# Kernel tuning notes

Hardware: AMD Instinct MI355X
Metric: run time of the kernel (lower is better)

## Reference

```python
import jax, jax.numpy as jnp
import numpy as np

ALPHA = 4.0   # spikingjelly sigmoid surrogate alpha
TAU = 2.0
EPS = 1e-5
NUM_HEADS = 8

@jax.custom_vjp
def spike(x):
    return (x >= 0.0).astype(x.dtype)

def _spike_fwd(x):
    return spike(x), x

def _spike_bwd(x, g):
    s = jax.nn.sigmoid(ALPHA * x)
    return (g * ALPHA * s * (1.0 - s),)

spike.defvjp(_spike_fwd, _spike_bwd)

def lif(x):
    # Multi-step LIF over leading time axis T; hard reset to 0, detach_reset=True.
    def step(v, xt):
        h = v + (xt - v) / TAU
        s = spike(h - 1.0)
        v_new = (1.0 - jax.lax.stop_gradient(s)) * h
        return v_new, s
    _, out = jax.lax.scan(step, jnp.zeros_like(x[0]), x)
    return out

def bn(x, gamma, beta):
    # x: (T*B, N, D). torch applies BatchNorm1d on (T*B, D, N): per-channel-D
    # batch stats over (T*B, N) dims (training mode, biased var).
    mean = x.mean(axis=(0, 1))
    var = x.var(axis=(0, 1))
    return (x - mean) * jax.lax.rsqrt(var + EPS) * gamma + beta

def proximity_mask(T):
    # assumed create_temporal_proximity_mask: weight decays with |i-j|
    idx = jnp.arange(T)
    return 1.0 / (1.0 + jnp.abs(idx[:, None] - idx[None, :]).astype(jnp.float32))

def _branch(x, W, g, b, T, B, H, d):
    D = H * d
    y = bn(x.reshape(T * B, -1, D) @ W.T, g, b)
    return lif(y.reshape(T, B, -1, H, d))  # (T,B,N,H,d)

def _forward(q, kv, Wq, gq, bq, Wk, gk, bk, Wv, gv, bv, Wp, gp, bp):
    T, B, N, D = q.shape
    H = NUM_HEADS
    d = D // H
    scale = D ** (-0.5)
    mask = proximity_mask(T)  # (T,T)

    qh = _branch(q, Wq, gq, bq, T, B, H, d)   # (T,B,N,H,d)
    kh = _branch(kv, Wk, gk, bk, T, B, H, d)  # (T,B,N,H,d)
    vh = _branch(kv, Wv, gv, bv, T, B, H, d)  # (T,B,N,H,d)

    # torch: k,v transposed over (time, token) axes before matmul.
    # scores[x,b,h,i,j] = sum_d q[x,b,i,h,d] * k[j,b,x,h,d]
    scores = jnp.einsum('xbihd,jbxhd->xbhij', qh, kh)
    scores = scores * mask[None, None, None, :, :]
    # z[x,b,h,i,d] = sum_j scores[x,b,h,i,j] * v[j,b,x,h,d]
    z = jnp.einsum('xbhij,jbxhd->xbhid', scores, vh) * scale

    # permute(3,1,0,2,4) -> (i=N, B, x=T, H, d); reshape to (T,B,T,D)
    z = z.transpose(3, 1, 0, 2, 4).reshape(T, B, T, D)
    z = lif(z)  # attn_lif

    y = z.reshape(T * B, T, D) @ Wp.T
    y = bn(y, gp, bp).reshape(T, B, T, D)
    y = lif(y)  # proj_lif; dropout is identity (eval)
    return y

def setup_inputs() -> dict:
    T, B, N, D = 64, 8, 64, 384
    key = jax.random.key(0)
    ks = jax.random.split(key, 6)
    w = lambda k: (jax.random.normal(k, (D, D), dtype=jnp.float32) * 0.02)
    return {
        'q': jax.random.normal(ks[0], (T, B, N, D), dtype=jnp.float32),
        'kv': jax.random.normal(ks[1], (T, B, N, D), dtype=jnp.float32),
        'Wq': w(ks[2]), 'gq': jnp.ones((D,), jnp.float32), 'bq': jnp.zeros((D,), jnp.float32),
        'Wk': w(ks[3]), 'gk': jnp.ones((D,), jnp.float32), 'bk': jnp.zeros((D,), jnp.float32),
        'Wv': w(ks[4]), 'gv': jnp.ones((D,), jnp.float32), 'bv': jnp.zeros((D,), jnp.float32),
        'Wp': w(ks[5]), 'gp': jnp.ones((D,), jnp.float32), 'bp': jnp.zeros((D,), jnp.float32),
    }

def reference(q, kv, Wq, gq, bq, Wk, gk, bk, Wv, gv, bv, Wp, gp, bp):
    return _forward(q, kv, Wq, gq, bq, Wk, gk, bk, Wv, gv, bv, Wp, gp, bp)
```

## Files before the change

kernel.cpp:

```cpp
#include <hip/hip_runtime.h>

typedef unsigned char u8;
typedef unsigned short u16;
typedef unsigned int u32;
typedef unsigned long long u64;
typedef __attribute__((ext_vector_type(8))) short s16x8;
typedef __attribute__((ext_vector_type(4))) float f32x4;

#define T_DIM 64
#define B_DIM 8
#define N_DIM 64
#define D_DIM 384
#define H_DIM 8
#define HD 48
#define M_ROWS 32768
#define CH 196608
#define STATS_BLOCKS 256

#define IMG_PER_KSTEP 16384
#define IMG_PER_NTILE (12 * IMG_PER_KSTEP)
#define IMG_PER_W (3 * IMG_PER_NTILE)

__device__ __forceinline__ void split8(const float* e, int4& o1, int4& o2, int4& o3) {
  u16 h1[8], h2[8], h3[8];
#pragma unroll
  for (int i = 0; i < 8; ++i) {
    const float x = e[i];
    const u32 b = __float_as_uint(x);
    h1[i] = (u16)(b >> 16);
    const float x1 = __uint_as_float(b & 0xFFFF0000u);
    const float r1 = x - x1;
    const u32 c = __float_as_uint(r1);
    h2[i] = (u16)(c >> 16);
    const float x2 = __uint_as_float(c & 0xFFFF0000u);
    const float r2 = r1 - x2;
    h3[i] = (u16)(__float_as_uint(r2) >> 16);
  }
  o1 = make_int4((int)((u32)h1[0] | ((u32)h1[1] << 16)), (int)((u32)h1[2] | ((u32)h1[3] << 16)),
                 (int)((u32)h1[4] | ((u32)h1[5] << 16)), (int)((u32)h1[6] | ((u32)h1[7] << 16)));
  o2 = make_int4((int)((u32)h2[0] | ((u32)h2[1] << 16)), (int)((u32)h2[2] | ((u32)h2[3] << 16)),
                 (int)((u32)h2[4] | ((u32)h2[5] << 16)), (int)((u32)h2[6] | ((u32)h2[7] << 16)));
  o3 = make_int4((int)((u32)h3[0] | ((u32)h3[1] << 16)), (int)((u32)h3[2] | ((u32)h3[3] << 16)),
                 (int)((u32)h3[4] | ((u32)h3[5] << 16)), (int)((u32)h3[6] | ((u32)h3[7] << 16)));
}

__device__ __forceinline__ void split8_2(const float* e, int4& o1, int4& o2) {
  u16 h1[8], h2[8];
#pragma unroll
  for (int i = 0; i < 8; ++i) {
    const float x = e[i];
    const u32 b = __float_as_uint(x);
    h1[i] = (u16)(b >> 16);
    const float x1 = __uint_as_float(b & 0xFFFF0000u);
    const float r1 = x - x1;
    h2[i] = (u16)(__float_as_uint(r1) >> 16);
  }
  o1 = make_int4((int)((u32)h1[0] | ((u32)h1[1] << 16)), (int)((u32)h1[2] | ((u32)h1[3] << 16)),
                 (int)((u32)h1[4] | ((u32)h1[5] << 16)), (int)((u32)h1[6] | ((u32)h1[7] << 16)));
  o2 = make_int4((int)((u32)h2[0] | ((u32)h2[1] << 16)), (int)((u32)h2[2] | ((u32)h2[3] << 16)),
                 (int)((u32)h2[4] | ((u32)h2[5] << 16)), (int)((u32)h2[6] | ((u32)h2[7] << 16)));
}

__device__ __forceinline__ void split1(float xx, u16& a, u16& b2, u16& c) {
  const u32 u = __float_as_uint(xx);
  a = (u16)(u >> 16);
  const float x1 = __uint_as_float(u & 0xFFFF0000u);
  const float r1 = xx - x1;
  const u32 u2 = __float_as_uint(r1);
  b2 = (u16)(u2 >> 16);
  const float x2 = __uint_as_float(u2 & 0xFFFF0000u);
  const float r2 = r1 - x2;
  c = (u16)(__float_as_uint(r2) >> 16);
}

__device__ __forceinline__ u64 packmask48(const u8* p) {
  const int4 r0 = ((const int4*)p)[0];
  const int4 r1 = ((const int4*)p)[1];
  const int4 r2 = ((const int4*)p)[2];
  u32 wv[12] = {(u32)r0.x, (u32)r0.y, (u32)r0.z, (u32)r0.w,
                (u32)r1.x, (u32)r1.y, (u32)r1.z, (u32)r1.w,
                (u32)r2.x, (u32)r2.y, (u32)r2.z, (u32)r2.w};
  u64 bits = 0;
#pragma unroll
  for (int w = 0; w < 12; ++w) {
    const u32 u = wv[w];
    const u32 nib = (u & 1u) | ((u >> 7) & 2u) | ((u >> 14) & 4u) | ((u >> 21) & 8u);
    bits |= (u64)nib << (w * 4);
  }
  return bits;
}

__global__ __launch_bounds__(256) void prep_w(const float* __restrict__ W0,
                                              const float* __restrict__ W1,
                                              const float* __restrict__ W2,
                                              const float* __restrict__ W3,
                                              char* __restrict__ img) {
  const int widx = blockIdx.x & 3;
  const int nt = blockIdx.x >> 2;
  const float* W = (widx == 0) ? W0 : (widx == 1) ? W1 : (widx == 2) ? W2 : W3;
  char* base = img + (size_t)widx * IMG_PER_W + (size_t)nt * IMG_PER_NTILE;
  const int tid = threadIdx.x;
  const int nr = tid >> 1;
  const int kh = tid & 1;
  for (int ks = 0; ks < 12; ++ks) {
    const float* src = W + (size_t)(nt * 128 + nr) * D_DIM + ks * 32 + kh * 16;
    float4 v0 = ((const float4*)src)[0];
    float4 v1 = ((const float4*)src)[1];
    float4 v2 = ((const float4*)src)[2];
    float4 v3 = ((const float4*)src)[3];
    float e[16] = {v0.x, v0.y, v0.z, v0.w, v1.x, v1.y, v1.z, v1.w,
                   v2.x, v2.y, v2.z, v2.w, v3.x, v3.y, v3.z, v3.w};
    int4* dst = (int4*)(base + (size_t)ks * IMG_PER_KSTEP);
#pragma unroll
    for (int sub = 0; sub < 2; ++sub) {
      const int kc = kh * 2 + sub;
      int4 o1, o2, o3;
      split8(e + sub * 8, o1, o2, o3);
      dst[(0 * 4 + kc) * 128 + (nr ^ kc)] = o1;
      dst[(1 * 4 + kc) * 128 + (nr ^ kc)] = o2;
    }
  }
}

template <int ASPL>
__global__ __launch_bounds__(256) void gemm_bn(const void* __restrict__ Ain,
                                               const char* __restrict__ imgW,
                                               float* __restrict__ C,
                                               double* __restrict__ part) {
  constexpr int ABYTES = ASPL * 8192;
  __shared__ __align__(16) char shraw[ABYTES + 16384];
  int4* AchW = (int4*)shraw;
  int4* BchW = (int4*)(shraw + ABYTES);
  const s16x8* AchR = (const s16x8*)shraw;
  const s16x8* BchR = (const s16x8*)(shraw + ABYTES);

  const int tid = threadIdx.x;
  const int lane = tid & 63;
  const int w = tid >> 6;
  const int wm = w >> 1, wn = w & 1;
  const int lr = lane & 15;
  const int kcL = lane >> 4;

  const int wgid = blockIdx.x;
  const int xcdSlot = wgid & 7;
  const int inner = wgid >> 3;
  const int ntx = inner % 3;
  const int by = (inner / 3) * 8 + xcdSlot;
  const int bn = ntx * 128;
  const int bm = by * 128;

  const int4* imgI = (const int4*)(imgW + (size_t)ntx * IMG_PER_NTILE);

  int axc[4], bxc[4];
#pragma unroll
  for (int f = 0; f < 4; ++f) {
    axc[f] = kcL * 128 + ((wm * 64 + f * 16 + lr) ^ kcL);
    bxc[f] = kcL * 128 + ((wn * 64 + f * 16 + lr) ^ kcL);
  }

  float4 a0, a1, a2, a3;
  int4 za0, za1;
  int4 b0, b1, b2, b3;

  const int arow = tid >> 1, akh = tid & 1;
  const int c0 = tid, c1 = tid + 256;

#define LOADA(ks)                                                             \
  do {                                                                        \
    if (ASPL == 2) {                                                          \
      const float* ap = (const float*)Ain + (size_t)(bm + arow) * D_DIM +     \
                        (ks) * 32 + akh * 16;                                 \
      a0 = ((const float4*)ap)[0]; a1 = ((const float4*)ap)[1];               \
      a2 = ((const float4*)ap)[2]; a3 = ((const float4*)ap)[3];               \
    } else {                                                                  \
      const u16* zp = (const u16*)Ain;                                        \
      { const int kc = c0 >> 7, mp = c0 & 127;                                \
        za0 = *(const int4*)(zp + (size_t)(bm + (mp ^ kc)) * D_DIM +          \
                             (ks) * 32 + kc * 8); }                           \
      { const int kc = c1 >> 7, mp = c1 & 127;                                \
        za1 = *(const int4*)(zp + (size_t)(bm + (mp ^ kc)) * D_DIM +          \
                             (ks) * 32 + kc * 8); }                           \
    }                                                                         \
  } while (0)

#define LOADB(ks)                                                             \
  do {                                                                        \
    b0 = imgI[(ks) * 1024 + tid];                                             \
    b1 = imgI[(ks) * 1024 + tid + 256];                                       \
    b2 = imgI[(ks) * 1024 + tid + 512];                                       \
    b3 = imgI[(ks) * 1024 + tid + 768];                                       \
  } while (0)

#define WRITES()                                                              \
  do {                                                                        \
    if (ASPL == 2) {                                                          \
      float e0[8] = {a0.x, a0.y, a0.z, a0.w, a1.x, a1.y, a1.z, a1.w};         \
      float e1[8] = {a2.x, a2.y, a2.z, a2.w, a3.x, a3.y, a3.z, a3.w};         \
      int4 o1, o2;                                                            \
      { const int kc = akh * 2;                                               \
        split8_2(e0, o1, o2);                                                 \
        AchW[0 * 512 + kc * 128 + (arow ^ kc)] = o1;                          \
        AchW[1 * 512 + kc * 128 + (arow ^ kc)] = o2; }                        \
      { const int kc = akh * 2 + 1;                                           \
        split8_2(e1, o1, o2);                                                 \
        AchW[0 * 512 + kc * 128 + (arow ^ kc)] = o1;                          \
        AchW[1 * 512 + kc * 128 + (arow ^ kc)] = o2; }                        \
    } else {                                                                  \
      AchW[c0] = za0; AchW[c1] = za1;                                         \
    }                                                                         \
    BchW[tid] = b0; BchW[tid + 256] = b1;                                     \
    BchW[tid + 512] = b2; BchW[tid + 768] = b3;                               \
  } while (0)

  f32x4 acc[4][4] = {};

  LOADA(0); LOADB(0);
  WRITES();
  __syncthreads();

  for (int ks = 0; ks < 12; ++ks) {
    if (ks < 11) { LOADA(ks + 1); LOADB(ks + 1); }
    s16x8 af[ASPL][4];
#pragma unroll
    for (int s = 0; s < ASPL; ++s)
#pragma unroll
      for (int fm = 0; fm < 4; ++fm) af[s][fm] = AchR[s * 512 + axc[fm]];
#pragma unroll
    for (int fn = 0; fn < 4; ++fn) {
      const s16x8 bf0 = BchR[bxc[fn]];
      const s16x8 bf1 = BchR[512 + bxc[fn]];
      if (ASPL == 2) {
#pragma unroll
        for (int fm = 0; fm < 4; ++fm)
          acc[fm][fn] = __builtin_amdgcn_mfma_f32_16x16x32_bf16(af[ASPL - 1][fm], bf0, acc[fm][fn], 0, 0, 0);
      }
#pragma unroll
      for (int fm = 0; fm < 4; ++fm)
        acc[fm][fn] = __builtin_amdgcn_mfma_f32_16x16x32_bf16(af[0][fm], bf1, acc[fm][fn], 0, 0, 0);
#pragma unroll
      for (int fm = 0; fm < 4; ++fm)
        acc[fm][fn] = __builtin_amdgcn_mfma_f32_16x16x32_bf16(af[0][fm], bf0, acc[fm][fn], 0, 0, 0);
    }
    __syncthreads();
    if (ks < 11) { WRITES(); __syncthreads(); }
  }
#undef LOADA
#undef LOADB
#undef WRITES

#pragma unroll
  for (int fm = 0; fm < 4; ++fm)
#pragma unroll
    for (int fn = 0; fn < 4; ++fn) {
      const int row = bm + wm * 64 + fm * 16 + kcL * 4;
      const int col = bn + wn * 64 + fn * 16 + lr;
#pragma unroll
      for (int r = 0; r < 4; ++r)
        C[(size_t)(row + r) * D_DIM + col] = acc[fm][fn][r];
    }

  double* red = (double*)shraw;
#pragma unroll
  for (int fn = 0; fn < 4; ++fn) {
    const int col = wn * 64 + fn * 16 + lr;
    const int rg = wm * 4 + kcL;
    double s = 0.0, qd = 0.0;
#pragma unroll
    for (int fm = 0; fm < 4; ++fm)
#pragma unroll
      for (int r = 0; r < 4; ++r) {
        const double v = (double)acc[fm][fn][r];
        s += v;
        qd += v * v;
      }
    red[(rg * 128 + col) * 2 + 0] = s;
    red[(rg * 128 + col) * 2 + 1] = qd;
  }
  __syncthreads();
  if (tid < 128) {
    double S = 0.0, Q = 0.0;
#pragma unroll
    for (int rg = 0; rg < 8; ++rg) {
      S += red[(rg * 128 + tid) * 2 + 0];
      Q += red[(rg * 128 + tid) * 2 + 1];
    }
    const size_t pidx = ((size_t)by * D_DIM + bn + tid) * 2;
    part[pidx + 0] = S;
    part[pidx + 1] = Q;
  }
}

__global__ void bn_stats_final(const double* __restrict__ part,
                               const float* __restrict__ gamma,
                               const float* __restrict__ beta,
                               float* __restrict__ ss) {
  const int c = blockIdx.x * 64 + threadIdx.x;
  double s = 0.0, q = 0.0;
  for (int b = 0; b < STATS_BLOCKS; ++b) {
    s += part[((size_t)b * D_DIM + c) * 2 + 0];
    q += part[((size_t)b * D_DIM + c) * 2 + 1];
  }
  const double n = (double)M_ROWS;
  const double mean = s / n;
  const double var = q / n - mean * mean;
  const double rstd = 1.0 / sqrt(var + 1e-5);
  const double sc = (double)gamma[c] * rstd;
  ss[c * 2 + 0] = (float)sc;
  ss[c * 2 + 1] = (float)((double)beta[c] - mean * sc);
}

template <int MODE>
__global__ __launch_bounds__(256) void lif_kernel(float* Y,
                                                  const float* __restrict__ ss,
                                                  u8* __restrict__ spikes) {
  const int c = blockIdx.x * 256 + threadIdx.x;
  const int dd = c % D_DIM;
  const float scale = ss[dd * 2 + 0];
  const float shift = ss[dd * 2 + 1];
  float v = 0.0f;
  for (int t0 = 0; t0 < T_DIM; t0 += 8) {
    float xs[8];
#pragma unroll
    for (int u = 0; u < 8; ++u) xs[u] = Y[(size_t)(t0 + u) * CH + c];
#pragma unroll
    for (int u = 0; u < 8; ++u) {
      const float xv = xs[u] * scale + shift;
      const float hh = v + (xv - v) * 0.5f;
      const float sp = (hh >= 1.0f) ? 1.0f : 0.0f;
      v = (1.0f - sp) * hh;
      if (MODE == 0)
        spikes[(size_t)(t0 + u) * CH + c] = (u8)sp;
      else
        Y[(size_t)(t0 + u) * CH + c] = sp;
    }
  }
}

__global__ __launch_bounds__(256) void attn_kernel(const u8* __restrict__ qs,
                                                   const u8* __restrict__ ks,
                                                   const u8* __restrict__ vs,
                                                   u16* __restrict__ z) {
  const int gid = blockIdx.x;
  const int hg = (gid & 1) * 4;
  const int b = (gid >> 1) & 7;
  const int x = gid >> 4;
  const int w = threadIdx.x >> 6;
  const int h = hg + w;
  const int lane = threadIdx.x & 63;

  union Slab {
    struct { u64 qm[64]; u64 km[64]; float maskT[64]; u16 vt[48][80]; } a;
    float zl[64][50];
  };
  __shared__ Slab sh[4];
  Slab& S = sh[w];

  {
    const u8* qp = qs + ((size_t)((x * B_DIM + b) * N_DIM + lane)) * D_DIM + h * HD;
    S.a.qm[lane] = packmask48(qp);
    const size_t koff = ((size_t)((lane * B_DIM + b) * N_DIM + x)) * D_DIM + h * HD;
    S.a.km[lane] = packmask48(ks + koff);
    const u8* vp = vs + koff;
    const int4 r0 = ((const int4*)vp)[0];
    const int4 r1 = ((const int4*)vp)[1];
    const int4 r2 = ((const int4*)vp)[2];
    u32 vw[12] = {(u32)r0.x, (u32)r0.y, (u32)r0.z, (u32)r0.w,
                  (u32)r1.x, (u32)r1.y, (u32)r1.z, (u32)r1.w,
                  (u32)r2.x, (u32)r2.y, (u32)r2.z, (u32)r2.w};
#pragma unroll
    for (int ww = 0; ww < 12; ++ww) {
      const u32 u = vw[ww];
#pragma unroll
      for (int e = 0; e < 4; ++e)
        S.a.vt[ww * 4 + e][lane] = ((u >> (8 * e)) & 1u) ? (u16)0x3F80 : (u16)0;
    }
    S.a.maskT[lane] = 1.0f / (float)(1 + lane);
  }
  __syncthreads();

  const int lr = lane & 15;
  const int lg = lane >> 4;
  f32x4 acc[4][3] = {};

  for (int ksi = 0; ksi < 2; ++ksi) {
    const int j0 = lg * 8 + ksi * 32;
    s16x8 bf[3];
#pragma unroll
    for (int nf = 0; nf < 3; ++nf)
      bf[nf] = *(const s16x8*)&S.a.vt[lr + nf * 16][j0];
    s16x8 af[3][4];
#pragma unroll
    for (int mf = 0; mf < 4; ++mf) {
      const int i = lr + mf * 16;
      const u64 qi = S.a.qm[i];
      union { u32 w[4]; s16x8 v; } p1, p2, p3;
#pragma unroll
      for (int pp = 0; pp < 4; ++pp) {
        u16 aa[2], bb[2], cc[2];
#pragma unroll
        for (int e = 0; e < 2; ++e) {
          const int j = j0 + pp * 2 + e;
          const int cnt = __popcll(qi & S.a.km[j]);
          int ad = i - j;
          if (ad < 0) ad = -ad;
          const float sv = (float)cnt * S.a.maskT[ad];
          split1(sv, aa[e], bb[e], cc[e]);
        }
        p1.w[pp] = (u32)aa[0] | ((u32)aa[1] << 16);
        p2.w[pp] = (u32)bb[0] | ((u32)bb[1] << 16);
        p3.w[pp] = (u32)cc[0] | ((u32)cc[1] << 16);
      }
      af[0][mf] = p1.v;
      af[1][mf] = p2.v;
      af[2][mf] = p3.v;
    }
#pragma unroll
    for (int spi = 0; spi < 3; ++spi) {
      const int sp = 2 - spi;
#pragma unroll
      for (int nf = 0; nf < 3; ++nf)
#pragma unroll
        for (int mf = 0; mf < 4; ++mf)
          acc[mf][nf] = __builtin_amdgcn_mfma_f32_16x16x32_bf16(af[sp][mf], bf[nf],
                                                                acc[mf][nf], 0, 0, 0);
    }
  }
  __syncthreads();

  const float kScale = 0.05103103630798287f;
#pragma unroll
  for (int mf = 0; mf < 4; ++mf)
#pragma unroll
    for (int nf = 0; nf < 3; ++nf)
#pragma unroll
      for (int r = 0; r < 4; ++r)
        S.zl[mf * 16 + lg * 4 + r][lr + nf * 16] = acc[mf][nf][r] * kScale;
  __syncthreads();

  if (lane < HD) {
    float v = 0.0f;
    for (int i0 = 0; i0 < 64; i0 += 8) {
      float zv[8];
#pragma unroll
      for (int u = 0; u < 8; ++u) zv[u] = S.zl[i0 + u][lane];
#pragma unroll
      for (int u = 0; u < 8; ++u) {
        const float hh = v + (zv[u] - v) * 0.5f;
        const u16 sp16 = (hh >= 1.0f) ? (u16)0x3F80 : (u16)0;
        v = (hh >= 1.0f) ? 0.0f : hh;
        z[((size_t)(((i0 + u) * B_DIM + b) * T_DIM + x)) * D_DIM + h * HD + lane] = sp16;
      }
    }
  }
}

extern "C" void kernel_launch(void* const* d_in, const int* in_sizes, int n_in,
                              void* d_out, int out_size, void* d_ws, size_t ws_size,
                              hipStream_t stream) {
  const float* q  = (const float*)d_in[0];
  const float* kv = (const float*)d_in[1];
  const float* Wq = (const float*)d_in[2];
  const float* gq = (const float*)d_in[3];
  const float* bq = (const float*)d_in[4];
  const float* Wk = (const float*)d_in[5];
  const float* gk = (const float*)d_in[6];
  const float* bk = (const float*)d_in[7];
  const float* Wv = (const float*)d_in[8];
  const float* gv = (const float*)d_in[9];
  const float* bv = (const float*)d_in[10];
  const float* Wp = (const float*)d_in[11];
  const float* gp = (const float*)d_in[12];
  const float* bp = (const float*)d_in[13];
  float* out = (float*)d_out;
  char* ws = (char*)d_ws;

  float* Ybuf  = (float*)(ws + 0);
  u16*   Zb    = (u16*)(ws + 0);
  double* part = (double*)(ws + 50331648ull);
  float* ss    = (float*)(ws + 51904512ull);
  u8* qsb      = (u8*)(ws + 51907584ull);
  u8* ksb      = (u8*)(ws + 64490496ull);
  u8* vsb      = (u8*)(ws + 77073408ull);
  char* Wimg   = (char*)(ws + 89656320ull);

  const int GBLK = 768;

  prep_w<<<12, 256, 0, stream>>>(Wq, Wk, Wv, Wp, Wimg);

  gemm_bn<2><<<GBLK, 256, 0, stream>>>(q, Wimg + 0 * (size_t)IMG_PER_W, Ybuf, part);
  bn_stats_final<<<6, 64, 0, stream>>>(part, gq, bq, ss);
  lif_kernel<0><<<CH / 256, 256, 0, stream>>>(Ybuf, ss, qsb);

  gemm_bn<2><<<GBLK, 256, 0, stream>>>(kv, Wimg + 1 * (size_t)IMG_PER_W, Ybuf, part);
  bn_stats_final<<<6, 64, 0, stream>>>(part, gk, bk, ss);
  lif_kernel<0><<<CH / 256, 256, 0, stream>>>(Ybuf, ss, ksb);

  gemm_bn<2><<<GBLK, 256, 0, stream>>>(kv, Wimg + 2 * (size_t)IMG_PER_W, Ybuf, part);
  bn_stats_final<<<6, 64, 0, stream>>>(part, gv, bv, ss);
  lif_kernel<0><<<CH / 256, 256, 0, stream>>>(Ybuf, ss, vsb);

  attn_kernel<<<T_DIM * B_DIM * 2, 256, 0, stream>>>(qsb, ksb, vsb, Zb);

  gemm_bn<1><<<GBLK, 256, 0, stream>>>(Zb, Wimg + 3 * (size_t)IMG_PER_W, out, part);
  bn_stats_final<<<6, 64, 0, stream>>>(part, gp, bp, ss);
  lif_kernel<2><<<CH / 256, 256, 0, stream>>>(out, ss, (u8*)nullptr);
}
```

Baseline: 257.1 us.

## Load A fragments directly to registers and double-buffer B tiles in GEMM

The fp32-input GEMM now has each lane load its own A fragment rows from global memory and split them to bf16 hi/lo in registers, skipping the LDS staging of A. B tiles are double-buffered in LDS, which removes one barrier per k-step. The Zb-input GEMM gets its own kernel that double-buffers both A and B. The trade-off is more LDS per block and less coalesced A loads, since each lane reads 32-byte row segments.

```diff
diff --git a/kernel.cpp b/kernel.cpp
--- a/kernel.cpp
+++ b/kernel.cpp
@@ -20,6 +20,8 @@
 #define IMG_PER_KSTEP 16384
 #define IMG_PER_NTILE (12 * IMG_PER_KSTEP)
 #define IMG_PER_W (3 * IMG_PER_NTILE)
+
+union I4S { int4 i; s16x8 v; };
 
 __device__ __forceinline__ void split8(const float* e, int4& o1, int4& o2, int4& o3) {
   u16 h1[8], h2[8], h3[8];
@@ -122,17 +124,20 @@
   }
 }
 
-template <int ASPL>
-__global__ __launch_bounds__(256) void gemm_bn(const void* __restrict__ Ain,
-                                               const char* __restrict__ imgW,
-                                               float* __restrict__ C,
-                                               double* __restrict__ part) {
-  constexpr int ABYTES = ASPL * 8192;
-  __shared__ __align__(16) char shraw[ABYTES + 16384];
-  int4* AchW = (int4*)shraw;
-  int4* BchW = (int4*)(shraw + ABYTES);
-  const s16x8* AchR = (const s16x8*)shraw;
-  const s16x8* BchR = (const s16x8*)(shraw + ABYTES);
+__device__ __forceinline__ void decode_wg(int wgid, int& ntx, int& by) {
+  const int xcdSlot = wgid & 7;
+  const int inner = wgid >> 3;
+  ntx = inner % 3;
+  by = (inner / 3) * 8 + xcdSlot;
+}
+
+__global__ __launch_bounds__(256) void gemm_bn2(const float* __restrict__ A,
+                                                const char* __restrict__ imgW,
+                                                float* __restrict__ C,
+                                                double* __restrict__ part) {
+  __shared__ __align__(16) char shraw[32768];
+  int4* BchW = (int4*)shraw;
+  const s16x8* BchR = (const s16x8*)shraw;
 
   const int tid = threadIdx.x;
   const int lane = tid & 63;
@@ -141,49 +146,48 @@
   const int lr = lane & 15;
   const int kcL = lane >> 4;
 
-  const int wgid = blockIdx.x;
-  const int xcdSlot = wgid & 7;
-  const int inner = wgid >> 3;
-  const int ntx = inner % 3;
-  const int by = (inner / 3) * 8 + xcdSlot;
+  int ntx, by;
+  decode_wg(blockIdx.x, ntx, by);
   const int bn = ntx * 128;
   const int bm = by * 128;
 
   const int4* imgI = (const int4*)(imgW + (size_t)ntx * IMG_PER_NTILE);
 
-  int axc[4], bxc[4];
-#pragma unroll
-  for (int f = 0; f < 4; ++f) {
-    axc[f] = kcL * 128 + ((wm * 64 + f * 16 + lr) ^ kcL);
+  int bxc[4];
+#pragma unroll
+  for (int f = 0; f < 4; ++f)
     bxc[f] = kcL * 128 + ((wn * 64 + f * 16 + lr) ^ kcL);
-  }
-
-  float4 a0, a1, a2, a3;
-  int4 za0, za1;
+
+  const float* aBase = A + (size_t)(bm + wm * 64 + lr) * D_DIM + kcL * 8;
+
+  float4 ast[4][2];
+  s16x8 af0[4], af1[4];
   int4 b0, b1, b2, b3;
 
-  const int arow = tid >> 1, akh = tid & 1;
-  const int c0 = tid, c1 = tid + 256;
-
-#define LOADA(ks)                                                             \
-  do {                                                                        \
-    if (ASPL == 2) {                                                          \
-      const float* ap = (const float*)Ain + (size_t)(bm + arow) * D_DIM +     \
-                        (ks) * 32 + akh * 16;                                 \
-      a0 = ((const float4*)ap)[0]; a1 = ((const float4*)ap)[1];               \
-      a2 = ((const float4*)ap)[2]; a3 = ((const float4*)ap)[3];               \
-    } else {                                                                  \
-      const u16* zp = (const u16*)Ain;                                        \
-      { const int kc = c0 >> 7, mp = c0 & 127;                                \
-        za0 = *(const int4*)(zp + (size_t)(bm + (mp ^ kc)) * D_DIM +          \
-                             (ks) * 32 + kc * 8); }                           \
-      { const int kc = c1 >> 7, mp = c1 & 127;                                \
-        za1 = *(const int4*)(zp + (size_t)(bm + (mp ^ kc)) * D_DIM +          \
-                             (ks) * 32 + kc * 8); }                           \
+#define LOADA2(ks)                                                            \
+  do {                                                                        \
+    _Pragma("unroll")                                                         \
+    for (int f = 0; f < 4; ++f) {                                             \
+      const float* p = aBase + (size_t)f * (16 * D_DIM) + (ks) * 32;          \
+      ast[f][0] = *(const float4*)p;                                          \
+      ast[f][1] = *(const float4*)(p + 4);                                    \
     }                                                                         \
   } while (0)
 
-#define LOADB(ks)                                                             \
+#define SPLITA2()                                                             \
+  do {                                                                        \
+    _Pragma("unroll")                                                         \
+    for (int f = 0; f < 4; ++f) {                                             \
+      float e[8] = {ast[f][0].x, ast[f][0].y, ast[f][0].z, ast[f][0].w,       \
+                    ast[f][1].x, ast[f][1].y, ast[f][1].z, ast[f][1].w};      \
+      int4 o1, o2;                                                            \
+      split8_2(e, o1, o2);                                                    \
+      I4S u1; u1.i = o1; af0[f] = u1.v;                                       \
+      I4S u2; u2.i = o2; af1[f] = u2.v;                                       \
+    }                                                                         \
+  } while (0)
+
+#define LOADB2(ks)                                                            \
   do {                                                                        \
     b0 = imgI[(ks) * 1024 + tid];                                             \
     b1 = imgI[(ks) * 1024 + tid + 256];                                       \
@@ -191,62 +195,50 @@
     b3 = imgI[(ks) * 1024 + tid + 768];                                       \
   } while (0)
 
-#define WRITES()                                                              \
-  do {                                                                        \
-    if (ASPL == 2) {                                                          \
-      float e0[8] = {a0.x, a0.y, a0.z, a0.w, a1.x, a1.y, a1.z, a1.w};         \
-      float e1[8] = {a2.x, a2.y, a2.z, a2.w, a3.x, a3.y, a3.z, a3.w};         \
-      int4 o1, o2;                                                            \
-      { const int kc = akh * 2;                                               \
-        split8_2(e0, o1, o2);                                                 \
-        AchW[0 * 512 + kc * 128 + (arow ^ kc)] = o1;                          \
-        AchW[1 * 512 + kc * 128 + (arow ^ kc)] = o2; }                        \
-      { const int kc = akh * 2 + 1;                                           \
-        split8_2(e1, o1, o2);                                                 \
-        AchW[0 * 512 + kc * 128 + (arow ^ kc)] = o1;                          \
-        AchW[1 * 512 + kc * 128 + (arow ^ kc)] = o2; }                        \
-    } else {                                                                  \
-      AchW[c0] = za0; AchW[c1] = za1;                                         \
-    }                                                                         \
-    BchW[tid] = b0; BchW[tid + 256] = b1;                                     \
-    BchW[tid + 512] = b2; BchW[tid + 768] = b3;                               \
+#define WRITEB2(buf)                                                          \
+  do {                                                                        \
+    BchW[(buf) * 1024 + tid] = b0;                                            \
+    BchW[(buf) * 1024 + tid + 256] = b1;                                      \
+    BchW[(buf) * 1024 + tid + 512] = b2;                                      \
+    BchW[(buf) * 1024 + tid + 768] = b3;                                      \
   } while (0)
 
   f32x4 acc[4][4] = {};
 
-  LOADA(0); LOADB(0);
-  WRITES();
-  __syncthreads();
-
+  LOADB2(0);
+  WRITEB2(0);
+  LOADA2(0);
+  SPLITA2();
+  __syncthreads();
+
+  int cur = 0;
   for (int ks = 0; ks < 12; ++ks) {
-    if (ks < 11) { LOADA(ks + 1); LOADB(ks + 1); }
-    s16x8 af[ASPL][4];
-#pragma unroll
-    for (int s = 0; s < ASPL; ++s)
-#pragma unroll
-      for (int fm = 0; fm < 4; ++fm) af[s][fm] = AchR[s * 512 + axc[fm]];
+    if (ks < 11) { LOADA2(ks + 1); LOADB2(ks + 1); }
 #pragma unroll
     for (int fn = 0; fn < 4; ++fn) {
-      const s16x8 bf0 = BchR[bxc[fn]];
-      const s16x8 bf1 = BchR[512 + bxc[fn]];
-      if (ASPL == 2) {
-#pragma unroll
-        for (int fm = 0; fm < 4; ++fm)
-          acc[fm][fn] = __builtin_amdgcn_mfma_f32_16x16x32_bf16(af[ASPL - 1][fm], bf0, acc[fm][fn], 0, 0, 0);
-      }
+      const s16x8 bf0 = BchR[cur * 1024 + bxc[fn]];
+      const s16x8 bf1 = BchR[cur * 1024 + 512 + bxc[fn]];
 #pragma unroll
       for (int fm = 0; fm < 4; ++fm)
-        acc[fm][fn] = __builtin_amdgcn_mfma_f32_16x16x32_bf16(af[0][fm], bf1, acc[fm][fn], 0, 0, 0);
+        acc[fm][fn] = __builtin_amdgcn_mfma_f32_16x16x32_bf16(af1[fm], bf0, acc[fm][fn], 0, 0, 0);
 #pragma unroll
       for (int fm = 0; fm < 4; ++fm)
-        acc[fm][fn] = __builtin_amdgcn_mfma_f32_16x16x32_bf16(af[0][fm], bf0, acc[fm][fn], 0, 0, 0);
-    }
-    __syncthreads();
-    if (ks < 11) { WRITES(); __syncthreads(); }
-  }
-#undef LOADA
-#undef LOADB
-#undef WRITES
+        acc[fm][fn] = __builtin_amdgcn_mfma_f32_16x16x32_bf16(af0[fm], bf1, acc[fm][fn], 0, 0, 0);
+#pragma unroll
+      for (int fm = 0; fm < 4; ++fm)
+        acc[fm][fn] = __builtin_amdgcn_mfma_f32_16x16x32_bf16(af0[fm], bf0, acc[fm][fn], 0, 0, 0);
+    }
+    if (ks < 11) {
+      SPLITA2();
+      WRITEB2(cur ^ 1);
+      __syncthreads();
+      cur ^= 1;
+    }
+  }
+#undef LOADA2
+#undef SPLITA2
+#undef LOADB2
+#undef WRITEB2
 
 #pragma unroll
   for (int fm = 0; fm < 4; ++fm)
@@ -259,6 +251,154 @@
         C[(size_t)(row + r) * D_DIM + col] = acc[fm][fn][r];
     }
 
+  __syncthreads();
+  double* red = (double*)shraw;
+#pragma unroll
+  for (int fn = 0; fn < 4; ++fn) {
+    const int col = wn * 64 + fn * 16 + lr;
+    const int rg = wm * 4 + kcL;
+    double s = 0.0, qd = 0.0;
+#pragma unroll
+    for (int fm = 0; fm < 4; ++fm)
+#pragma unroll
+      for (int r = 0; r < 4; ++r) {
+        const double v = (double)acc[fm][fn][r];
+        s += v;
+        qd += v * v;
+      }
+    red[(rg * 128 + col) * 2 + 0] = s;
+    red[(rg * 128 + col) * 2 + 1] = qd;
+  }
+  __syncthreads();
+  if (tid < 128) {
+    double S = 0.0, Q = 0.0;
+#pragma unroll
+    for (int rg = 0; rg < 8; ++rg) {
+      S += red[(rg * 128 + tid) * 2 + 0];
+      Q += red[(rg * 128 + tid) * 2 + 1];
+    }
+    const size_t pidx = ((size_t)by * D_DIM + bn + tid) * 2;
+    part[pidx + 0] = S;
+    part[pidx + 1] = Q;
+  }
+}
+
+__global__ __launch_bounds__(256) void gemm_bn1(const u16* __restrict__ Zb,
+                                                const char* __restrict__ imgW,
+                                                float* __restrict__ C,
+                                                double* __restrict__ part) {
+  __shared__ __align__(16) char shraw[49152];
+  int4* BchW = (int4*)shraw;
+  const s16x8* BchR = (const s16x8*)shraw;
+  int4* AchW = (int4*)shraw + 2048;
+  const s16x8* AchR = (const s16x8*)shraw + 2048;
+
+  const int tid = threadIdx.x;
+  const int lane = tid & 63;
+  const int w = tid >> 6;
+  const int wm = w >> 1, wn = w & 1;
+  const int lr = lane & 15;
+  const int kcL = lane >> 4;
+
+  int ntx, by;
+  decode_wg(blockIdx.x, ntx, by);
+  const int bn = ntx * 128;
+  const int bm = by * 128;
+
+  const int4* imgI = (const int4*)(imgW + (size_t)ntx * IMG_PER_NTILE);
+
+  int axc[4], bxc[4];
+#pragma unroll
+  for (int f = 0; f < 4; ++f) {
+    axc[f] = kcL * 128 + ((wm * 64 + f * 16 + lr) ^ kcL);
+    bxc[f] = kcL * 128 + ((wn * 64 + f * 16 + lr) ^ kcL);
+  }
+
+  int4 za0, za1;
+  int4 b0, b1, b2, b3;
+  const int c0 = tid, c1 = tid + 256;
+
+#define LOADA1(ks)                                                            \
+  do {                                                                        \
+    { const int kc = c0 >> 7, mp = c0 & 127;                                  \
+      za0 = *(const int4*)(Zb + (size_t)(bm + (mp ^ kc)) * D_DIM +            \
+                           (ks) * 32 + kc * 8); }                             \
+    { const int kc = c1 >> 7, mp = c1 & 127;                                  \
+      za1 = *(const int4*)(Zb + (size_t)(bm + (mp ^ kc)) * D_DIM +            \
+                           (ks) * 32 + kc * 8); }                             \
+  } while (0)
+
+#define WRITEA1(buf)                                                          \
+  do {                                                                        \
+    AchW[(buf) * 512 + c0] = za0;                                             \
+    AchW[(buf) * 512 + c1] = za1;                                             \
+  } while (0)
+
+#define LOADB1(ks)                                                            \
+  do {                                                                        \
+    b0 = imgI[(ks) * 1024 + tid];                                             \
+    b1 = imgI[(ks) * 1024 + tid + 256];                                       \
+    b2 = imgI[(ks) * 1024 + tid + 512];                                       \
+    b3 = imgI[(ks) * 1024 + tid + 768];                                       \
+  } while (0)
+
+#define WRITEB1(buf)                                                          \
+  do {                                                                        \
+    BchW[(buf) * 1024 + tid] = b0;                                            \
+    BchW[(buf) * 1024 + tid + 256] = b1;                                      \
+    BchW[(buf) * 1024 + tid + 512] = b2;                                      \
+    BchW[(buf) * 1024 + tid + 768] = b3;                                      \
+  } while (0)
+
+  f32x4 acc[4][4] = {};
+
+  LOADA1(0);
+  LOADB1(0);
+  WRITEA1(0);
+  WRITEB1(0);
+  __syncthreads();
+
+  int cur = 0;
+  for (int ks = 0; ks < 12; ++ks) {
+    if (ks < 11) { LOADA1(ks + 1); LOADB1(ks + 1); }
+    s16x8 af[4];
+#pragma unroll
+    for (int fm = 0; fm < 4; ++fm) af[fm] = AchR[cur * 512 + axc[fm]];
+#pragma unroll
+    for (int fn = 0; fn < 4; ++fn) {
+      const s16x8 bf0 = BchR[cur * 1024 + bxc[fn]];
+      const s16x8 bf1 = BchR[cur * 1024 + 512 + bxc[fn]];
+#pragma unroll
+      for (int fm = 0; fm < 4; ++fm)
+        acc[fm][fn] = __builtin_amdgcn_mfma_f32_16x16x32_bf16(af[fm], bf1, acc[fm][fn], 0, 0, 0);
+#pragma unroll
+      for (int fm = 0; fm < 4; ++fm)
+        acc[fm][fn] = __builtin_amdgcn_mfma_f32_16x16x32_bf16(af[fm], bf0, acc[fm][fn], 0, 0, 0);
+    }
+    if (ks < 11) {
+      WRITEA1(cur ^ 1);
+      WRITEB1(cur ^ 1);
+      __syncthreads();
+      cur ^= 1;
+    }
+  }
+#undef LOADA1
+#undef WRITEA1
+#undef LOADB1
+#undef WRITEB1
+
+#pragma unroll
+  for (int fm = 0; fm < 4; ++fm)
+#pragma unroll
+    for (int fn = 0; fn < 4; ++fn) {
+      const int row = bm + wm * 64 + fm * 16 + kcL * 4;
+      const int col = bn + wn * 64 + fn * 16 + lr;
+#pragma unroll
+      for (int r = 0; r < 4; ++r)
+        C[(size_t)(row + r) * D_DIM + col] = acc[fm][fn][r];
+    }
+
+  __syncthreads();
   double* red = (double*)shraw;
 #pragma unroll
   for (int fn = 0; fn < 4; ++fn) {
@@ -487,21 +627,21 @@
 
   prep_w<<<12, 256, 0, stream>>>(Wq, Wk, Wv, Wp, Wimg);
 
-  gemm_bn<2><<<GBLK, 256, 0, stream>>>(q, Wimg + 0 * (size_t)IMG_PER_W, Ybuf, part);
+  gemm_bn2<<<GBLK, 256, 0, stream>>>(q, Wimg + 0 * (size_t)IMG_PER_W, Ybuf, part);
   bn_stats_final<<<6, 64, 0, stream>>>(part, gq, bq, ss);
   lif_kernel<0><<<CH / 256, 256, 0, stream>>>(Ybuf, ss, qsb);
 
-  gemm_bn<2><<<GBLK, 256, 0, stream>>>(kv, Wimg + 1 * (size_t)IMG_PER_W, Ybuf, part);
+  gemm_bn2<<<GBLK, 256, 0, stream>>>(kv, Wimg + 1 * (size_t)IMG_PER_W, Ybuf, part);
   bn_stats_final<<<6, 64, 0, stream>>>(part, gk, bk, ss);
   lif_kernel<0><<<CH / 256, 256, 0, stream>>>(Ybuf, ss, ksb);
 
-  gemm_bn<2><<<GBLK, 256, 0, stream>>>(kv, Wimg + 2 * (size_t)IMG_PER_W, Ybuf, part);
+  gemm_bn2<<<GBLK, 256, 0, stream>>>(kv, Wimg + 2 * (size_t)IMG_PER_W, Ybuf, part);
   bn_stats_final<<<6, 64, 0, stream>>>(part, gv, bv, ss);
   lif_kernel<0><<<CH / 256, 256, 0, stream>>>(Ybuf, ss, vsb);
 
   attn_kernel<<<T_DIM * B_DIM * 2, 256, 0, stream>>>(qsb, ksb, vsb, Zb);
 
-  gemm_bn<1><<<GBLK, 256, 0, stream>>>(Zb, Wimg + 3 * (size_t)IMG_PER_W, out, part);
+  gemm_bn1<<<GBLK, 256, 0, stream>>>(Zb, Wimg + 3 * (size_t)IMG_PER_W, out, part);
   bn_stats_final<<<6, 64, 0, stream>>>(part, gp, bp, ss);
   lif_kernel<2><<<CH / 256, 256, 0, stream>>>(out, ss, (u8*)nullptr);
 }
```

After: 339.0 us. 1.32x slower.
